# Optimization experiments

Measured on AMD Instinct MI355X. Metric: run time of the kernel, lower is better.

Reference implementation:

```python
import jax, jax.numpy as jnp
import numpy as np

D_MODEL = 1024
EXPANDED = 1024  # d_model * expansion_factor(1.0)
K = 3
EPS = 1e-8


def rms_norm(x, w, eps=EPS):
    return x * jax.lax.rsqrt(jnp.mean(x * x, axis=-1, keepdims=True) + eps) * w


def setup_inputs() -> dict:
    key = jax.random.key(0)
    ks = jax.random.split(key, 8)
    b, t = 4, 4096
    u = jax.random.normal(ks[0], (b, t, D_MODEL), dtype=jnp.float32)
    s_in = 1.0 / np.sqrt(D_MODEL)
    s_out = 1.0 / np.sqrt(EXPANDED)
    W_in = jax.random.uniform(ks[1], (2 * EXPANDED, D_MODEL), jnp.float32, -s_in, s_in)
    b_in = jax.random.uniform(ks[2], (2 * EXPANDED,), jnp.float32, -s_in, s_in)
    in_norm_w = jnp.ones((2 * EXPANDED,), jnp.float32)
    s_conv = 1.0 / np.sqrt(K)  # groups=expanded_dim -> fan_in = K
    conv_w = jax.random.uniform(ks[3], (EXPANDED, 1, K), jnp.float32, -s_conv, s_conv)
    conv_b = jax.random.uniform(ks[4], (EXPANDED,), jnp.float32, -s_conv, s_conv)
    W_out = jax.random.uniform(ks[5], (D_MODEL, EXPANDED), jnp.float32, -s_out, s_out)
    b_out = jax.random.uniform(ks[6], (D_MODEL,), jnp.float32, -s_out, s_out)
    out_norm_w = jnp.ones((D_MODEL,), jnp.float32)
    return {
        "u": u, "W_in": W_in, "b_in": b_in, "in_norm_w": in_norm_w,
        "conv_w": conv_w, "conv_b": conv_b,
        "W_out": W_out, "b_out": b_out, "out_norm_w": out_norm_w,
    }


def reference(u, W_in, b_in, in_norm_w, conv_w, conv_b, W_out, b_out, out_norm_w):
    # in_proj + RMSNorm
    xv = rms_norm(jnp.einsum('btd,ed->bte', u, W_in) + b_in, in_norm_w)  # [b,t,2E]
    x, v = jnp.split(xv, 2, axis=-1)  # each [b,t,E]
    # depthwise 'same' conv along time: NCH layout
    x_f = jnp.transpose(x, (0, 2, 1))  # [b,E,t]
    pad = (K - 1) // 2
    y = jax.lax.conv_general_dilated(
        x_f, conv_w, window_strides=(1,), padding=[(pad, pad)],
        dimension_numbers=('NCH', 'OIH', 'NCH'), feature_group_count=EXPANDED)
    y = y + conv_b[None, :, None]
    x_mixed = jnp.transpose(y, (0, 2, 1))  # [b,t,E]
    gated = v * x_mixed
    out = rms_norm(jnp.einsum('bte,de->btd', gated, W_out) + b_out, out_norm_w)
    return out
```

## Files before the change

kernel.cpp:

```cpp
#include <hip/hip_runtime.h>

#define BT    16384
#define TSEQ  4096
#define DM    1024
#define EXP   1024
#define N1    2048
#define KDIM  1024
#define NKT   32
#define EPSV  1e-8f

typedef __bf16 bf16x8 __attribute__((ext_vector_type(8)));
typedef float f32x16 __attribute__((ext_vector_type(16)));
typedef unsigned short u16x8 __attribute__((ext_vector_type(8)));

#define AS1CAST(p) ((__attribute__((address_space(1))) void*)(p))
#define AS3CAST(p) ((__attribute__((address_space(3))) void*)(p))

__device__ __forceinline__ unsigned short f2bf(float f) {
    unsigned int u = __float_as_uint(f);
    u += 0x7fffu + ((u >> 16) & 1u);
    return (unsigned short)(u >> 16);
}

__global__ __launch_bounds__(256) void k_f2bf3(const float* __restrict__ i0, unsigned short* __restrict__ o0, int n0,
                                               const float* __restrict__ i1, unsigned short* __restrict__ o1, int n1,
                                               const float* __restrict__ i2, unsigned short* __restrict__ o2, int n2,
                                               float* __restrict__ ssq) {
    int i = blockIdx.x * 256 + threadIdx.x;
    const float* in; unsigned short* out;
    if (i < n0)                { in = i0; out = o0; }
    else if (i < n0 + n1)      { in = i1; out = o1; i -= n0; }
    else if (i < n0 + n1 + n2) { in = i2; out = o2; i -= n0 + n1; }
    else {
        i -= n0 + n1 + n2;
        if (i < 2 * BT / 4) ((float4*)ssq)[i] = make_float4(0.f, 0.f, 0.f, 0.f);
        return;
    }
    float4 v = ((const float4*)in)[i];
    ushort4 o;
    o.x = f2bf(v.x); o.y = f2bf(v.y); o.z = f2bf(v.z); o.w = f2bf(v.w);
    ((ushort4*)out)[i] = o;
}

template <int BF16_OUT, int NT>
__device__ __forceinline__ void gemm_body(const unsigned short* __restrict__ A,
                                          const unsigned short* __restrict__ Bw,
                                          const float* __restrict__ bias,
                                          unsigned short* __restrict__ Cb,
                                          float* __restrict__ Cf,
                                          float* __restrict__ ssq,
                                          int N) {
    __shared__ __align__(16) char smem[73728];

    const int tid  = threadIdx.x;
    const int lane = tid & 63;
    const int w    = tid >> 6;
    const int ln   = lane & 31;
    const int hi   = lane >> 5;

    const int L   = blockIdx.x;
    const int mt  = ((L >> 3) / NT) * 8 + (L & 7);
    const int nt  = (L >> 3) & (NT - 1);
    const int row0 = mt * 256, col0 = nt * 128;

    const int rA = tid >> 2;
    const int qS = ((tid & 3) - (tid >> 4)) & 3;
    const unsigned short* aSrc = A  + (size_t)(row0 + rA) * KDIM + qS * 8;
    const unsigned short* bSrc = Bw + (size_t)(col0 + rA) * KDIM + qS * 8;

    f32x16 acc[2][4] = {};

    auto stage = [&](int kt, unsigned short* sA, unsigned short* sB) {
#pragma unroll
        for (int b = 0; b < 4; ++b)
            __builtin_amdgcn_global_load_lds(AS1CAST(aSrc + (size_t)b * 64 * KDIM + kt * 32),
                                             AS3CAST(&sA[(b * 256 + w * 64) * 8]), 16, 0, 0);
#pragma unroll
        for (int b = 0; b < 2; ++b)
            __builtin_amdgcn_global_load_lds(AS1CAST(bSrc + (size_t)b * 64 * KDIM + kt * 32),
                                             AS3CAST(&sB[(b * 256 + w * 64) * 8]), 16, 0, 0);
    };
    auto compute = [&](const unsigned short* sA, const unsigned short* sB) {
#pragma unroll
        for (int ks = 0; ks < 2; ++ks) {
            const int sw = ((ks * 2 + hi + (ln >> 2)) & 3) * 8;
            bf16x8 aF[2], bF[4];
#pragma unroll
            for (int i = 0; i < 2; ++i)
                aF[i] = *(const bf16x8*)&sA[(w * 64 + i * 32 + ln) * 32 + sw];
#pragma unroll
            for (int j = 0; j < 4; ++j)
                bF[j] = *(const bf16x8*)&sB[(j * 32 + ln) * 32 + sw];
            __builtin_amdgcn_s_setprio(1);
#pragma unroll
            for (int i = 0; i < 2; ++i)
#pragma unroll
                for (int j = 0; j < 4; ++j)
                    acc[i][j] = __builtin_amdgcn_mfma_f32_32x32x16_bf16(
                        aF[i], bF[j], acc[i][j], 0, 0, 0);
            __builtin_amdgcn_s_setprio(0);
        }
    };

    unsigned short* A0 = (unsigned short*)smem;
    unsigned short* B0 = (unsigned short*)(smem + 16384);
    unsigned short* A1 = (unsigned short*)(smem + 24576);
    unsigned short* B1 = (unsigned short*)(smem + 40960);
    unsigned short* A2 = (unsigned short*)(smem + 49152);
    unsigned short* B2 = (unsigned short*)(smem + 65536);

    stage(0, A0, B0);
    stage(1, A1, B1);
    for (int kt = 0; kt < NKT - 1; ++kt) {
        asm volatile("s_waitcnt vmcnt(6)" ::: "memory");
        __builtin_amdgcn_s_barrier();
        if (kt + 2 < NKT) stage(kt + 2, A2, B2);
        compute(A0, B0);
        unsigned short* tA = A0; A0 = A1; A1 = A2; A2 = tA;
        unsigned short* tB = B0; B0 = B1; B1 = B2; B2 = tB;
    }
    asm volatile("s_waitcnt vmcnt(0)" ::: "memory");
    __builtin_amdgcn_s_barrier();
    compute(A0, B0);

    const int c0 = col0 + ln;
    float bs[4];
#pragma unroll
    for (int j = 0; j < 4; ++j) bs[j] = bias[c0 + j * 32];

    __syncthreads();
    float* scr = (float*)smem;

#pragma unroll
    for (int i = 0; i < 2; ++i) {
        const int lr0 = w * 64 + i * 32 + 4 * hi;
#pragma unroll
        for (int reg = 0; reg < 16; ++reg) {
            const int lr = lr0 + (reg & 3) + 8 * (reg >> 2);
            const int gm = row0 + lr;
            float v[4]; float p = 0.f;
#pragma unroll
            for (int j = 0; j < 4; ++j) {
                v[j] = acc[i][j][reg] + bs[j];
                p += v[j] * v[j];
            }
            scr[lr * 33 + ln] = p;
            size_t base = (size_t)gm * N + c0;
#pragma unroll
            for (int j = 0; j < 4; ++j) {
                if (BF16_OUT) Cb[base + j * 32] = f2bf(v[j]);
                else          Cf[base + j * 32] = v[j];
            }
        }
    }
    __syncthreads();
    float s = 0.f;
#pragma unroll
    for (int c = 0; c < 32; ++c) s += scr[tid * 33 + c];
    atomicAdd(&ssq[row0 + tid], s);
}

__global__ __launch_bounds__(256, 2) void k_gemm_in(const unsigned short* __restrict__ A,
                                                    const unsigned short* __restrict__ Bw,
                                                    const float* __restrict__ bias,
                                                    unsigned short* __restrict__ Cb,
                                                    float* __restrict__ ssq) {
    gemm_body<1, 16>(A, Bw, bias, Cb, nullptr, ssq, N1);
}

__global__ __launch_bounds__(256, 2) void k_gemm_out(const unsigned short* __restrict__ A,
                                                     const unsigned short* __restrict__ Bw,
                                                     const float* __restrict__ bias,
                                                     float* __restrict__ Cf,
                                                     float* __restrict__ ssq) {
    gemm_body<0, 8>(A, Bw, bias, nullptr, Cf, ssq, DM);
}

__global__ __launch_bounds__(256) void k_conv_gate(const unsigned short* __restrict__ z,
                                                   const float* __restrict__ ssq1,
                                                   const float* __restrict__ inw,
                                                   const float* __restrict__ cw,
                                                   const float* __restrict__ cb,
                                                   unsigned short* __restrict__ g) {
    const int tok = blockIdx.x * 2 + (threadIdx.x >> 7);
    const int e8  = (threadIdx.x & 127) * 8;
    const int t   = tok & (TSEQ - 1);

    const float rs0 = rsqrtf(ssq1[tok] * (1.0f / N1) + EPSV);
    const int tm = (t > 0) ? tok - 1 : tok;
    const int tp = (t < TSEQ - 1) ? tok + 1 : tok;
    const float rsm = (t > 0) ? rsqrtf(ssq1[tm] * (1.0f / N1) + EPSV) : 0.0f;
    const float rsp = (t < TSEQ - 1) ? rsqrtf(ssq1[tp] * (1.0f / N1) + EPSV) : 0.0f;

    bf16x8 xm = *(const bf16x8*)(z + (size_t)tm * N1 + e8);
    bf16x8 x0 = *(const bf16x8*)(z + (size_t)tok * N1 + e8);
    bf16x8 xp = *(const bf16x8*)(z + (size_t)tp * N1 + e8);
    bf16x8 vv = *(const bf16x8*)(z + (size_t)tok * N1 + EXP + e8);

    u16x8 ov;
#pragma unroll
    for (int p = 0; p < 8; ++p) {
        const int e = e8 + p;
        const float we  = inw[e];
        const float wvv = inw[EXP + e];
        const float w0 = cw[e * 3], w1 = cw[e * 3 + 1], w2 = cw[e * 3 + 2];
        float y = w0 * ((float)xm[p] * rsm * we)
                + w1 * ((float)x0[p] * rs0 * we)
                + w2 * ((float)xp[p] * rsp * we)
                + cb[e];
        float vn = (float)vv[p] * rs0 * wvv;
        ov[p] = f2bf(vn * y);
    }
    *(u16x8*)(g + (size_t)tok * EXP + e8) = ov;
}

__global__ __launch_bounds__(256) void k_outnorm(float* __restrict__ o,
                                                 const float* __restrict__ ssq2,
                                                 const float* __restrict__ onw) {
    const int idx = blockIdx.x * 256 + threadIdx.x;
    const int tok = idx >> 8;
    const int d4  = (idx & 255) * 4;
    const float rs = rsqrtf(ssq2[tok] * (1.0f / DM) + EPSV);
    float4 v = ((float4*)o)[idx];
    float4 w = *(const float4*)(onw + d4);
    v.x *= rs * w.x; v.y *= rs * w.y; v.z *= rs * w.z; v.w *= rs * w.w;
    ((float4*)o)[idx] = v;
}

extern "C" void kernel_launch(void* const* d_in, const int* in_sizes, int n_in,
                              void* d_out, int out_size, void* d_ws, size_t ws_size,
                              hipStream_t stream) {
    const float* u     = (const float*)d_in[0];
    const float* W_in  = (const float*)d_in[1];
    const float* b_in  = (const float*)d_in[2];
    const float* inw   = (const float*)d_in[3];
    const float* cw    = (const float*)d_in[4];
    const float* cb    = (const float*)d_in[5];
    const float* W_out = (const float*)d_in[6];
    const float* b_out = (const float*)d_in[7];
    const float* onw   = (const float*)d_in[8];
    float* out = (float*)d_out;

    char* ws = (char*)d_ws;
    unsigned short* u_bf    = (unsigned short*)ws; ws += (size_t)BT * DM * 2;
    unsigned short* Win_bf  = (unsigned short*)ws; ws += (size_t)N1 * DM * 2;
    unsigned short* Wout_bf = (unsigned short*)ws; ws += (size_t)DM * EXP * 2;
    unsigned short* z_bf    = (unsigned short*)ws; ws += (size_t)BT * N1 * 2;
    unsigned short* g_bf    = (unsigned short*)ws; ws += (size_t)BT * EXP * 2;
    float* ssq1 = (float*)ws; ws += (size_t)BT * 4;
    float* ssq2 = (float*)ws; ws += (size_t)BT * 4;

    const int n0 = BT * DM / 4, n1c = N1 * DM / 4, n2c = DM * EXP / 4;
    const int ntot = n0 + n1c + n2c + 2 * BT / 4;
    k_f2bf3<<<(ntot + 255) / 256, 256, 0, stream>>>(u, u_bf, n0,
                                                    W_in, Win_bf, n1c,
                                                    W_out, Wout_bf, n2c,
                                                    ssq1);

    k_gemm_in<<<(BT / 256) * (N1 / 128), 256, 0, stream>>>(u_bf, Win_bf, b_in, z_bf, ssq1);

    k_conv_gate<<<BT / 2, 256, 0, stream>>>(z_bf, ssq1, inw, cw, cb, g_bf);

    k_gemm_out<<<(BT / 256) * (DM / 128), 256, 0, stream>>>(g_bf, Wout_bf, b_out, out, ssq2);

    k_outnorm<<<BT, 256, 0, stream>>>(out, ssq2, onw);

    (void)in_sizes; (void)n_in; (void)out_size; (void)ws_size;
}
```

Measured before the change: 299.6 us.

## Restructure GEMMs to 256x256 tiles with 8 waves and 16x16 MFMA

Both projection GEMMs move from 256x128 tiles on 4 waves to 256x256 tiles on 8 waves (512 threads), using 16x16x32 bf16 MFMAs and a 64-wide K step. Each K step is split into two halves whose global-to-LDS loads are interleaved with MFMA phases, with barriers between phases and a new XOR swizzle. The row sum-of-squares reduction now uses lane shuffles and per-row atomics instead of an LDS scratch pass. Larger tiles cut global and LDS traffic per flop, but the 128 KB of LDS and high register use limit occupancy and add more barriers.

After: 301.9 us. No clear change (+0.8%).

```diff
diff --git a/kernel.cpp b/kernel.cpp
--- a/kernel.cpp
+++ b/kernel.cpp
@@ -6,11 +6,11 @@
 #define EXP   1024
 #define N1    2048
 #define KDIM  1024
-#define NKT   32
+#define NKT   16
 #define EPSV  1e-8f
 
 typedef __bf16 bf16x8 __attribute__((ext_vector_type(8)));
-typedef float f32x16 __attribute__((ext_vector_type(16)));
+typedef float f32x4 __attribute__((ext_vector_type(4)));
 typedef unsigned short u16x8 __attribute__((ext_vector_type(8)));
 
 #define AS1CAST(p) ((__attribute__((address_space(1))) void*)(p))
@@ -42,7 +42,7 @@
     ((ushort4*)out)[i] = o;
 }
 
-template <int BF16_OUT, int NT>
+template <int BF16_OUT, int NTN>
 __device__ __forceinline__ void gemm_body(const unsigned short* __restrict__ A,
                                           const unsigned short* __restrict__ Bw,
                                           const float* __restrict__ bias,
@@ -50,130 +50,165 @@
                                           float* __restrict__ Cf,
                                           float* __restrict__ ssq,
                                           int N) {
-    __shared__ __align__(16) char smem[73728];
+    __shared__ __align__(16) char smem[131072];
 
     const int tid  = threadIdx.x;
     const int lane = tid & 63;
     const int w    = tid >> 6;
-    const int ln   = lane & 31;
-    const int hi   = lane >> 5;
+    const int wm   = w >> 2;
+    const int wn   = w & 3;
+    const int l15  = lane & 15;
+    const int l4   = lane >> 4;
 
     const int L   = blockIdx.x;
-    const int mt  = ((L >> 3) / NT) * 8 + (L & 7);
-    const int nt  = (L >> 3) & (NT - 1);
-    const int row0 = mt * 256, col0 = nt * 128;
-
-    const int rA = tid >> 2;
-    const int qS = ((tid & 3) - (tid >> 4)) & 3;
-    const unsigned short* aSrc = A  + (size_t)(row0 + rA) * KDIM + qS * 8;
-    const unsigned short* bSrc = Bw + (size_t)(col0 + rA) * KDIM + qS * 8;
-
-    f32x16 acc[2][4] = {};
-
-    auto stage = [&](int kt, unsigned short* sA, unsigned short* sB) {
-#pragma unroll
-        for (int b = 0; b < 4; ++b)
-            __builtin_amdgcn_global_load_lds(AS1CAST(aSrc + (size_t)b * 64 * KDIM + kt * 32),
-                                             AS3CAST(&sA[(b * 256 + w * 64) * 8]), 16, 0, 0);
+    const int cpx = (NTN * (BT / 256)) >> 3;
+    const int W   = (L & 7) * cpx + (L >> 3);
+    const int mt  = W / NTN, nt = W % NTN;
+    const int row0 = mt * 256, col0 = nt * 256;
+
+    const int rS = tid >> 2;
+    const int qS = (tid & 3) ^ ((tid >> 3) & 3);
+
+    auto stageA = [&](int T2, int kh) {
+        const unsigned short* src = A + (size_t)(row0 + rS) * KDIM + T2 * 64 + kh * 32 + qS * 8;
+        char* dst = smem + ((T2 & 1) * 32768 + kh * 16384) + tid * 16;
 #pragma unroll
         for (int b = 0; b < 2; ++b)
-            __builtin_amdgcn_global_load_lds(AS1CAST(bSrc + (size_t)b * 64 * KDIM + kt * 32),
-                                             AS3CAST(&sB[(b * 256 + w * 64) * 8]), 16, 0, 0);
+            __builtin_amdgcn_global_load_lds(AS1CAST(src + (size_t)b * 128 * KDIM),
+                                             AS3CAST(dst + b * 8192), 16, 0, 0);
     };
-    auto compute = [&](const unsigned short* sA, const unsigned short* sB) {
-#pragma unroll
-        for (int ks = 0; ks < 2; ++ks) {
-            const int sw = ((ks * 2 + hi + (ln >> 2)) & 3) * 8;
-            bf16x8 aF[2], bF[4];
-#pragma unroll
-            for (int i = 0; i < 2; ++i)
-                aF[i] = *(const bf16x8*)&sA[(w * 64 + i * 32 + ln) * 32 + sw];
-#pragma unroll
-            for (int j = 0; j < 4; ++j)
-                bF[j] = *(const bf16x8*)&sB[(j * 32 + ln) * 32 + sw];
-            __builtin_amdgcn_s_setprio(1);
-#pragma unroll
-            for (int i = 0; i < 2; ++i)
-#pragma unroll
-                for (int j = 0; j < 4; ++j)
-                    acc[i][j] = __builtin_amdgcn_mfma_f32_32x32x16_bf16(
-                        aF[i], bF[j], acc[i][j], 0, 0, 0);
-            __builtin_amdgcn_s_setprio(0);
-        }
+    auto stageB = [&](int T2, int kh) {
+        const unsigned short* src = Bw + (size_t)(col0 + rS) * KDIM + T2 * 64 + kh * 32 + qS * 8;
+        char* dst = smem + (65536 + (T2 & 1) * 32768 + kh * 16384) + tid * 16;
+#pragma unroll
+        for (int b = 0; b < 2; ++b)
+            __builtin_amdgcn_global_load_lds(AS1CAST(src + (size_t)b * 128 * KDIM),
+                                             AS3CAST(dst + b * 8192), 16, 0, 0);
     };
 
-    unsigned short* A0 = (unsigned short*)smem;
-    unsigned short* B0 = (unsigned short*)(smem + 16384);
-    unsigned short* A1 = (unsigned short*)(smem + 24576);
-    unsigned short* B1 = (unsigned short*)(smem + 40960);
-    unsigned short* A2 = (unsigned short*)(smem + 49152);
-    unsigned short* B2 = (unsigned short*)(smem + 65536);
-
-    stage(0, A0, B0);
-    stage(1, A1, B1);
-    for (int kt = 0; kt < NKT - 1; ++kt) {
-        asm volatile("s_waitcnt vmcnt(6)" ::: "memory");
-        __builtin_amdgcn_s_barrier();
-        if (kt + 2 < NKT) stage(kt + 2, A2, B2);
-        compute(A0, B0);
-        unsigned short* tA = A0; A0 = A1; A1 = A2; A2 = tA;
-        unsigned short* tB = B0; B0 = B1; B1 = B2; B2 = tB;
+    const int pslot = (l4 ^ ((l15 >> 1) & 3)) * 16;
+    const int aL = (wm * 128 + l15) * 64 + pslot;
+    const int bL = (wn * 64 + l15) * 64 + pslot;
+
+    f32x4 acc[8][4] = {};
+
+    stageA(0, 0); stageB(0, 0);
+    stageA(0, 1); stageB(0, 1);
+    stageA(1, 0); stageB(1, 0);
+    asm volatile("s_waitcnt vmcnt(4)" ::: "memory");
+    __builtin_amdgcn_s_barrier();
+
+#pragma unroll 1
+    for (int T = 0; T < NKT; ++T) {
+        const char* Ab = smem + (T & 1) * 32768;
+        const char* Bb = smem + 65536 + (T & 1) * 32768;
+        bf16x8 aF[8], bF[4];
+
+#pragma unroll
+        for (int mr = 0; mr < 8; ++mr) aF[mr] = *(const bf16x8*)(Ab + aL + mr * 1024);
+        bF[0] = *(const bf16x8*)(Bb + bL);
+        bF[1] = *(const bf16x8*)(Bb + bL + 1024);
+        if (T + 1 < NKT) stageA(T + 1, 1);
+        __builtin_amdgcn_s_barrier();
+        asm volatile("s_waitcnt lgkmcnt(0)" ::: "memory");
+        __builtin_amdgcn_s_setprio(1);
+#pragma unroll
+        for (int mr = 0; mr < 8; ++mr) {
+            acc[mr][0] = __builtin_amdgcn_mfma_f32_16x16x32_bf16(aF[mr], bF[0], acc[mr][0], 0, 0, 0);
+            acc[mr][1] = __builtin_amdgcn_mfma_f32_16x16x32_bf16(aF[mr], bF[1], acc[mr][1], 0, 0, 0);
+        }
+        __builtin_amdgcn_s_setprio(0);
+        __builtin_amdgcn_s_barrier();
+
+        bF[2] = *(const bf16x8*)(Bb + bL + 2048);
+        bF[3] = *(const bf16x8*)(Bb + bL + 3072);
+        if (T + 1 < NKT) stageB(T + 1, 1);
+        __builtin_amdgcn_s_barrier();
+        asm volatile("s_waitcnt lgkmcnt(0)" ::: "memory");
+        __builtin_amdgcn_s_setprio(1);
+#pragma unroll
+        for (int mr = 0; mr < 8; ++mr) {
+            acc[mr][2] = __builtin_amdgcn_mfma_f32_16x16x32_bf16(aF[mr], bF[2], acc[mr][2], 0, 0, 0);
+            acc[mr][3] = __builtin_amdgcn_mfma_f32_16x16x32_bf16(aF[mr], bF[3], acc[mr][3], 0, 0, 0);
+        }
+        __builtin_amdgcn_s_setprio(0);
+        __builtin_amdgcn_s_barrier();
+
+#pragma unroll
+        for (int mr = 0; mr < 8; ++mr) aF[mr] = *(const bf16x8*)(Ab + 16384 + aL + mr * 1024);
+        bF[0] = *(const bf16x8*)(Bb + 16384 + bL);
+        bF[1] = *(const bf16x8*)(Bb + 16384 + bL + 1024);
+        if (T + 2 < NKT) stageA(T + 2, 0);
+        __builtin_amdgcn_s_barrier();
+        asm volatile("s_waitcnt lgkmcnt(0)" ::: "memory");
+        __builtin_amdgcn_s_setprio(1);
+#pragma unroll
+        for (int mr = 0; mr < 8; ++mr) {
+            acc[mr][0] = __builtin_amdgcn_mfma_f32_16x16x32_bf16(aF[mr], bF[0], acc[mr][0], 0, 0, 0);
+            acc[mr][1] = __builtin_amdgcn_mfma_f32_16x16x32_bf16(aF[mr], bF[1], acc[mr][1], 0, 0, 0);
+        }
+        __builtin_amdgcn_s_setprio(0);
+        __builtin_amdgcn_s_barrier();
+
+        bF[2] = *(const bf16x8*)(Bb + 16384 + bL + 2048);
+        bF[3] = *(const bf16x8*)(Bb + 16384 + bL + 3072);
+        if (T + 2 < NKT) stageB(T + 2, 0);
+        __builtin_amdgcn_s_barrier();
+        asm volatile("s_waitcnt lgkmcnt(0)" ::: "memory");
+        __builtin_amdgcn_s_setprio(1);
+#pragma unroll
+        for (int mr = 0; mr < 8; ++mr) {
+            acc[mr][2] = __builtin_amdgcn_mfma_f32_16x16x32_bf16(aF[mr], bF[2], acc[mr][2], 0, 0, 0);
+            acc[mr][3] = __builtin_amdgcn_mfma_f32_16x16x32_bf16(aF[mr], bF[3], acc[mr][3], 0, 0, 0);
+        }
+        __builtin_amdgcn_s_setprio(0);
+        if (T < NKT - 2) asm volatile("s_waitcnt vmcnt(4)" ::: "memory");
+        else             asm volatile("s_waitcnt vmcnt(0)" ::: "memory");
+        __builtin_amdgcn_s_barrier();
     }
-    asm volatile("s_waitcnt vmcnt(0)" ::: "memory");
-    __builtin_amdgcn_s_barrier();
-    compute(A0, B0);
-
-    const int c0 = col0 + ln;
-    float bs[4];
-#pragma unroll
-    for (int j = 0; j < 4; ++j) bs[j] = bias[c0 + j * 32];
-
-    __syncthreads();
-    float* scr = (float*)smem;
-
-#pragma unroll
-    for (int i = 0; i < 2; ++i) {
-        const int lr0 = w * 64 + i * 32 + 4 * hi;
-#pragma unroll
-        for (int reg = 0; reg < 16; ++reg) {
-            const int lr = lr0 + (reg & 3) + 8 * (reg >> 2);
-            const int gm = row0 + lr;
-            float v[4]; float p = 0.f;
-#pragma unroll
-            for (int j = 0; j < 4; ++j) {
-                v[j] = acc[i][j][reg] + bs[j];
-                p += v[j] * v[j];
+
+    const int c0 = col0 + wn * 64 + l15;
+    float bsv[4];
+#pragma unroll
+    for (int nr = 0; nr < 4; ++nr) bsv[nr] = bias[c0 + nr * 16];
+
+#pragma unroll
+    for (int mr = 0; mr < 8; ++mr) {
+#pragma unroll
+        for (int reg = 0; reg < 4; ++reg) {
+            const int gm = row0 + wm * 128 + mr * 16 + l4 * 4 + reg;
+            const size_t base = (size_t)gm * N + c0;
+            float p = 0.f;
+#pragma unroll
+            for (int nr = 0; nr < 4; ++nr) {
+                float v = acc[mr][nr][reg] + bsv[nr];
+                p += v * v;
+                if (BF16_OUT) Cb[base + nr * 16] = f2bf(v);
+                else          Cf[base + nr * 16] = v;
             }
-            scr[lr * 33 + ln] = p;
-            size_t base = (size_t)gm * N + c0;
-#pragma unroll
-            for (int j = 0; j < 4; ++j) {
-                if (BF16_OUT) Cb[base + j * 32] = f2bf(v[j]);
-                else          Cf[base + j * 32] = v[j];
-            }
+            p += __shfl_xor(p, 1);
+            p += __shfl_xor(p, 2);
+            p += __shfl_xor(p, 4);
+            p += __shfl_xor(p, 8);
+            if (l15 == 0) atomicAdd(&ssq[gm], p);
         }
     }
-    __syncthreads();
-    float s = 0.f;
-#pragma unroll
-    for (int c = 0; c < 32; ++c) s += scr[tid * 33 + c];
-    atomicAdd(&ssq[row0 + tid], s);
-}
-
-__global__ __launch_bounds__(256, 2) void k_gemm_in(const unsigned short* __restrict__ A,
+}
+
+__global__ __launch_bounds__(512, 2) void k_gemm_in(const unsigned short* __restrict__ A,
                                                     const unsigned short* __restrict__ Bw,
                                                     const float* __restrict__ bias,
                                                     unsigned short* __restrict__ Cb,
                                                     float* __restrict__ ssq) {
-    gemm_body<1, 16>(A, Bw, bias, Cb, nullptr, ssq, N1);
-}
-
-__global__ __launch_bounds__(256, 2) void k_gemm_out(const unsigned short* __restrict__ A,
+    gemm_body<1, 8>(A, Bw, bias, Cb, nullptr, ssq, N1);
+}
+
+__global__ __launch_bounds__(512, 2) void k_gemm_out(const unsigned short* __restrict__ A,
                                                      const unsigned short* __restrict__ Bw,
                                                      const float* __restrict__ bias,
                                                      float* __restrict__ Cf,
                                                      float* __restrict__ ssq) {
-    gemm_body<0, 8>(A, Bw, bias, nullptr, Cf, ssq, DM);
+    gemm_body<0, 4>(A, Bw, bias, nullptr, Cf, ssq, DM);
 }
 
 __global__ __launch_bounds__(256) void k_conv_gate(const unsigned short* __restrict__ z,
@@ -257,11 +292,11 @@
                                                     W_out, Wout_bf, n2c,
                                                     ssq1);
 
-    k_gemm_in<<<(BT / 256) * (N1 / 128), 256, 0, stream>>>(u_bf, Win_bf, b_in, z_bf, ssq1);
+    k_gemm_in<<<(BT / 256) * (N1 / 256), 512, 0, stream>>>(u_bf, Win_bf, b_in, z_bf, ssq1);
 
     k_conv_gate<<<BT / 2, 256, 0, stream>>>(z_bf, ssq1, inw, cw, cb, g_bf);
 
-    k_gemm_out<<<(BT / 256) * (DM / 128), 256, 0, stream>>>(g_bf, Wout_bf, b_out, out, ssq2);
+    k_gemm_out<<<(BT / 256) * (DM / 256), 512, 0, stream>>>(g_bf, Wout_bf, b_out, out, ssq2);
 
     k_outnorm<<<BT, 256, 0, stream>>>(out, ssq2, onw);
 
```

## Fuse output RMSNorm into a full-row output GEMM kernel

Applied to the files above, without the earlier changes.

Replaces the tiled output GEMM, its atomic sum-of-squares accumulation and the separate output-norm pass with one kernel. Each 512-thread block computes 64 complete rows across all 1024 output columns and reduces the row norms in shared memory before writing the normalized result once. This removes a full fp32 read/write pass over the output, the atomics and one launch. In exchange every block streams all of W_out from L2, uses about 136KB of LDS (one block per CU) and drops to a double-buffered pipeline that waits on all loads each step.

Result: slower. 305.9 us (+2.1%).

```diff
diff --git a/kernel.cpp b/kernel.cpp
--- a/kernel.cpp
+++ b/kernel.cpp
@@ -6,7 +6,7 @@
 #define EXP   1024
 #define N1    2048
 #define KDIM  1024
-#define NKT   32
+#define NKT2  (KDIM / 32)
 #define EPSV  1e-8f
 
 typedef __bf16 bf16x8 __attribute__((ext_vector_type(8)));
@@ -33,7 +33,7 @@
     else if (i < n0 + n1 + n2) { in = i2; out = o2; i -= n0 + n1; }
     else {
         i -= n0 + n1 + n2;
-        if (i < 2 * BT / 4) ((float4*)ssq)[i] = make_float4(0.f, 0.f, 0.f, 0.f);
+        if (i < BT / 4) ((float4*)ssq)[i] = make_float4(0.f, 0.f, 0.f, 0.f);
         return;
     }
     float4 v = ((const float4*)in)[i];
@@ -111,10 +111,10 @@
 
     stage(0, A0, B0);
     stage(1, A1, B1);
-    for (int kt = 0; kt < NKT - 1; ++kt) {
+    for (int kt = 0; kt < NKT2 - 1; ++kt) {
         asm volatile("s_waitcnt vmcnt(6)" ::: "memory");
         __builtin_amdgcn_s_barrier();
-        if (kt + 2 < NKT) stage(kt + 2, A2, B2);
+        if (kt + 2 < NKT2) stage(kt + 2, A2, B2);
         compute(A0, B0);
         unsigned short* tA = A0; A0 = A1; A1 = A2; A2 = tA;
         unsigned short* tB = B0; B0 = B1; B1 = B2; B2 = tB;
@@ -168,12 +168,122 @@
     gemm_body<1, 16>(A, Bw, bias, Cb, nullptr, ssq, N1);
 }
 
-__global__ __launch_bounds__(256, 2) void k_gemm_out(const unsigned short* __restrict__ A,
-                                                     const unsigned short* __restrict__ Bw,
-                                                     const float* __restrict__ bias,
-                                                     float* __restrict__ Cf,
-                                                     float* __restrict__ ssq) {
-    gemm_body<0, 8>(A, Bw, bias, nullptr, Cf, ssq, DM);
+__global__ __launch_bounds__(512, 2) void k_gemm_outn(const unsigned short* __restrict__ A,
+                                                      const unsigned short* __restrict__ Bw,
+                                                      const float* __restrict__ bias,
+                                                      const float* __restrict__ onw,
+                                                      float* __restrict__ O) {
+    __shared__ __align__(16) char smem[139264];
+
+    const int tid  = threadIdx.x;
+    const int lane = tid & 63;
+    const int w    = tid >> 6;
+    const int ln   = lane & 31;
+    const int hi   = lane >> 5;
+    const int row0 = blockIdx.x * 64;
+
+    const int rS = tid >> 2;
+    const int qS = ((tid & 3) - (tid >> 4)) & 3;
+    const unsigned short* aSrc = A  + (size_t)(row0 + (rS & 63)) * KDIM + qS * 8;
+    const unsigned short* bSrc = Bw + (size_t)rS * KDIM + qS * 8;
+
+    auto stage = [&](int kt, char* sA, char* sB) {
+        if (tid < 256)
+            __builtin_amdgcn_global_load_lds(AS1CAST(aSrc + kt * 32),
+                                             AS3CAST(sA + tid * 16), 16, 0, 0);
+#pragma unroll
+        for (int b = 0; b < 8; ++b)
+            __builtin_amdgcn_global_load_lds(AS1CAST(bSrc + (size_t)b * 128 * KDIM + kt * 32),
+                                             AS3CAST(sB + (b * 512 + tid) * 16), 16, 0, 0);
+    };
+
+    f32x16 acc[2][4] = {};
+
+    auto compute = [&](const char* sAc, const char* sBc) {
+        const unsigned short* sA = (const unsigned short*)sAc;
+        const unsigned short* sB = (const unsigned short*)sBc;
+#pragma unroll
+        for (int ks = 0; ks < 2; ++ks) {
+            const int sw = ((ks * 2 + hi + (ln >> 2)) & 3) * 8;
+            bf16x8 aF[2], bF[4];
+#pragma unroll
+            for (int i = 0; i < 2; ++i)
+                aF[i] = *(const bf16x8*)&sA[(i * 32 + ln) * 32 + sw];
+#pragma unroll
+            for (int j = 0; j < 4; ++j)
+                bF[j] = *(const bf16x8*)&sB[(w * 128 + j * 32 + ln) * 32 + sw];
+            __builtin_amdgcn_s_setprio(1);
+#pragma unroll
+            for (int i = 0; i < 2; ++i)
+#pragma unroll
+                for (int j = 0; j < 4; ++j)
+                    acc[i][j] = __builtin_amdgcn_mfma_f32_32x32x16_bf16(
+                        aF[i], bF[j], acc[i][j], 0, 0, 0);
+            __builtin_amdgcn_s_setprio(0);
+        }
+    };
+
+    char* A0 = smem;          char* B0 = smem + 4096;
+    char* A1 = smem + 69632;  char* B1 = smem + 73728;
+
+    stage(0, A0, B0);
+#pragma unroll 1
+    for (int T = 0; T < NKT2; ++T) {
+        asm volatile("s_waitcnt vmcnt(0)" ::: "memory");
+        __builtin_amdgcn_s_barrier();
+        if (T + 1 < NKT2) stage(T + 1, (T & 1) ? A0 : A1, (T & 1) ? B0 : B1);
+        compute((T & 1) ? A1 : A0, (T & 1) ? B1 : B0);
+    }
+
+    __syncthreads();
+    float* part = (float*)smem;
+
+    const int c0 = w * 128 + ln;
+    float bs[4], wn[4];
+#pragma unroll
+    for (int j = 0; j < 4; ++j) { bs[j] = bias[c0 + j * 32]; wn[j] = onw[c0 + j * 32]; }
+
+#pragma unroll
+    for (int i = 0; i < 2; ++i) {
+#pragma unroll
+        for (int reg = 0; reg < 16; ++reg) {
+            const int r = i * 32 + (reg & 3) + 8 * (reg >> 2) + 4 * hi;
+            float p = 0.f;
+#pragma unroll
+            for (int j = 0; j < 4; ++j) {
+                float v = acc[i][j][reg] + bs[j];
+                p += v * v;
+            }
+            p += __shfl_xor(p, 1);
+            p += __shfl_xor(p, 2);
+            p += __shfl_xor(p, 4);
+            p += __shfl_xor(p, 8);
+            p += __shfl_xor(p, 16);
+            if (ln == 0) part[r * 8 + w] = p;
+        }
+    }
+    __syncthreads();
+    if (tid < 64) {
+        float s = 0.f;
+#pragma unroll
+        for (int k = 0; k < 8; ++k) s += part[tid * 8 + k];
+        part[512 + tid] = rsqrtf(s * (1.0f / DM) + EPSV);
+    }
+    __syncthreads();
+    const float* rsv = part + 512;
+
+#pragma unroll
+    for (int i = 0; i < 2; ++i) {
+#pragma unroll
+        for (int reg = 0; reg < 16; ++reg) {
+            const int r = i * 32 + (reg & 3) + 8 * (reg >> 2) + 4 * hi;
+            const float rf = rsv[r];
+            const size_t base = (size_t)(row0 + r) * DM + c0;
+#pragma unroll
+            for (int j = 0; j < 4; ++j)
+                O[base + j * 32] = (acc[i][j][reg] + bs[j]) * rf * wn[j];
+        }
+    }
 }
 
 __global__ __launch_bounds__(256) void k_conv_gate(const unsigned short* __restrict__ z,
@@ -212,19 +322,6 @@
         ov[p] = f2bf(vn * y);
     }
     *(u16x8*)(g + (size_t)tok * EXP + e8) = ov;
-}
-
-__global__ __launch_bounds__(256) void k_outnorm(float* __restrict__ o,
-                                                 const float* __restrict__ ssq2,
-                                                 const float* __restrict__ onw) {
-    const int idx = blockIdx.x * 256 + threadIdx.x;
-    const int tok = idx >> 8;
-    const int d4  = (idx & 255) * 4;
-    const float rs = rsqrtf(ssq2[tok] * (1.0f / DM) + EPSV);
-    float4 v = ((float4*)o)[idx];
-    float4 w = *(const float4*)(onw + d4);
-    v.x *= rs * w.x; v.y *= rs * w.y; v.z *= rs * w.z; v.w *= rs * w.w;
-    ((float4*)o)[idx] = v;
 }
 
 extern "C" void kernel_launch(void* const* d_in, const int* in_sizes, int n_in,
@@ -248,10 +345,9 @@
     unsigned short* z_bf    = (unsigned short*)ws; ws += (size_t)BT * N1 * 2;
     unsigned short* g_bf    = (unsigned short*)ws; ws += (size_t)BT * EXP * 2;
     float* ssq1 = (float*)ws; ws += (size_t)BT * 4;
-    float* ssq2 = (float*)ws; ws += (size_t)BT * 4;
 
     const int n0 = BT * DM / 4, n1c = N1 * DM / 4, n2c = DM * EXP / 4;
-    const int ntot = n0 + n1c + n2c + 2 * BT / 4;
+    const int ntot = n0 + n1c + n2c + BT / 4;
     k_f2bf3<<<(ntot + 255) / 256, 256, 0, stream>>>(u, u_bf, n0,
                                                     W_in, Win_bf, n1c,
                                                     W_out, Wout_bf, n2c,
@@ -261,9 +357,7 @@
 
     k_conv_gate<<<BT / 2, 256, 0, stream>>>(z_bf, ssq1, inw, cw, cb, g_bf);
 
-    k_gemm_out<<<(BT / 256) * (DM / 128), 256, 0, stream>>>(g_bf, Wout_bf, b_out, out, ssq2);
-
-    k_outnorm<<<BT, 256, 0, stream>>>(out, ssq2, onw);
+    k_gemm_outn<<<BT / 64, 512, 0, stream>>>(g_bf, Wout_bf, b_out, onw, out);
 
     (void)in_sizes; (void)n_in; (void)out_size; (void)ws_size;
 }
```

## Fuse output RMSNorm into out-GEMM via last-block counter and remap conv blocks

Applied to the files above, without the earlier changes.

Removes the separate output-norm kernel. Each out-GEMM block bumps a per-row-tile atomic counter, and the last of the 8 column blocks for a 256-row tile reads the finished sum of squares and rescales that tile's rows in place. The counter array is zeroed alongside ssq in the conversion kernel. The conv_gate block index is also permuted so neighbouring blocks are spread across 8 groups, probably to improve XCD/cache locality. This saves a launch and one pass over the output, but the whole normalization of a tile now falls on a single block, and the out-GEMM's tile-to-block mapping has to match the mt formula used here.

Result: slower. 477.6 us (+59.4%).

```diff
diff --git a/kernel.cpp b/kernel.cpp
--- a/kernel.cpp
+++ b/kernel.cpp
@@ -6,7 +6,7 @@
 #define EXP   1024
 #define N1    2048
 #define KDIM  1024
-#define NKT   32
+#define NKT2  (KDIM / 32)
 #define EPSV  1e-8f
 
 typedef __bf16 bf16x8 __attribute__((ext_vector_type(8)));
@@ -33,7 +33,7 @@
     else if (i < n0 + n1 + n2) { in = i2; out = o2; i -= n0 + n1; }
     else {
         i -= n0 + n1 + n2;
-        if (i < 2 * BT / 4) ((float4*)ssq)[i] = make_float4(0.f, 0.f, 0.f, 0.f);
+        if (i < (2 * BT + 64) / 4) ((float4*)ssq)[i] = make_float4(0.f, 0.f, 0.f, 0.f);
         return;
     }
     float4 v = ((const float4*)in)[i];
@@ -111,10 +111,10 @@
 
     stage(0, A0, B0);
     stage(1, A1, B1);
-    for (int kt = 0; kt < NKT - 1; ++kt) {
+    for (int kt = 0; kt < NKT2 - 1; ++kt) {
         asm volatile("s_waitcnt vmcnt(6)" ::: "memory");
         __builtin_amdgcn_s_barrier();
-        if (kt + 2 < NKT) stage(kt + 2, A2, B2);
+        if (kt + 2 < NKT2) stage(kt + 2, A2, B2);
         compute(A0, B0);
         unsigned short* tA = A0; A0 = A1; A1 = A2; A2 = tA;
         unsigned short* tB = B0; B0 = B1; B1 = B2; B2 = tB;
@@ -172,8 +172,37 @@
                                                      const unsigned short* __restrict__ Bw,
                                                      const float* __restrict__ bias,
                                                      float* __restrict__ Cf,
-                                                     float* __restrict__ ssq) {
+                                                     float* __restrict__ ssq,
+                                                     const float* __restrict__ onw,
+                                                     int* __restrict__ cnt) {
     gemm_body<0, 8>(A, Bw, bias, nullptr, Cf, ssq, DM);
+
+    const int L   = blockIdx.x;
+    const int mt  = ((L >> 3) / 8) * 8 + (L & 7);
+    const int row0 = mt * 256;
+
+    __shared__ int done;
+    __shared__ float rsbuf[256];
+
+    __threadfence();
+    if (threadIdx.x == 0) done = atomicAdd(&cnt[mt], 1);
+    __syncthreads();
+    if (done != 7) return;
+
+    __threadfence();
+    rsbuf[threadIdx.x] = rsqrtf(ssq[row0 + threadIdx.x] * (1.0f / DM) + EPSV);
+    __syncthreads();
+
+    const float4 wv = ((const float4*)onw)[threadIdx.x];
+    float4* Of = (float4*)Cf;
+#pragma unroll 4
+    for (int r = 0; r < 256; ++r) {
+        const float rs = rsbuf[r];
+        const size_t idx = (size_t)(row0 + r) * 256 + threadIdx.x;
+        float4 v = Of[idx];
+        v.x *= rs * wv.x; v.y *= rs * wv.y; v.z *= rs * wv.z; v.w *= rs * wv.w;
+        Of[idx] = v;
+    }
 }
 
 __global__ __launch_bounds__(256) void k_conv_gate(const unsigned short* __restrict__ z,
@@ -182,7 +211,9 @@
                                                    const float* __restrict__ cw,
                                                    const float* __restrict__ cb,
                                                    unsigned short* __restrict__ g) {
-    const int tok = blockIdx.x * 2 + (threadIdx.x >> 7);
+    const int L   = blockIdx.x;
+    const int blk = (L & 7) * 1024 + (L >> 3);
+    const int tok = blk * 2 + (threadIdx.x >> 7);
     const int e8  = (threadIdx.x & 127) * 8;
     const int t   = tok & (TSEQ - 1);
 
@@ -212,19 +243,6 @@
         ov[p] = f2bf(vn * y);
     }
     *(u16x8*)(g + (size_t)tok * EXP + e8) = ov;
-}
-
-__global__ __launch_bounds__(256) void k_outnorm(float* __restrict__ o,
-                                                 const float* __restrict__ ssq2,
-                                                 const float* __restrict__ onw) {
-    const int idx = blockIdx.x * 256 + threadIdx.x;
-    const int tok = idx >> 8;
-    const int d4  = (idx & 255) * 4;
-    const float rs = rsqrtf(ssq2[tok] * (1.0f / DM) + EPSV);
-    float4 v = ((float4*)o)[idx];
-    float4 w = *(const float4*)(onw + d4);
-    v.x *= rs * w.x; v.y *= rs * w.y; v.z *= rs * w.z; v.w *= rs * w.w;
-    ((float4*)o)[idx] = v;
 }
 
 extern "C" void kernel_launch(void* const* d_in, const int* in_sizes, int n_in,
@@ -249,9 +267,10 @@
     unsigned short* g_bf    = (unsigned short*)ws; ws += (size_t)BT * EXP * 2;
     float* ssq1 = (float*)ws; ws += (size_t)BT * 4;
     float* ssq2 = (float*)ws; ws += (size_t)BT * 4;
+    int*   cnt  = (int*)ws;  ws += 64 * 4;
 
     const int n0 = BT * DM / 4, n1c = N1 * DM / 4, n2c = DM * EXP / 4;
-    const int ntot = n0 + n1c + n2c + 2 * BT / 4;
+    const int ntot = n0 + n1c + n2c + (2 * BT + 64) / 4;
     k_f2bf3<<<(ntot + 255) / 256, 256, 0, stream>>>(u, u_bf, n0,
                                                     W_in, Win_bf, n1c,
                                                     W_out, Wout_bf, n2c,
@@ -261,9 +280,7 @@
 
     k_conv_gate<<<BT / 2, 256, 0, stream>>>(z_bf, ssq1, inw, cw, cb, g_bf);
 
-    k_gemm_out<<<(BT / 256) * (DM / 128), 256, 0, stream>>>(g_bf, Wout_bf, b_out, out, ssq2);
-
-    k_outnorm<<<BT, 256, 0, stream>>>(out, ssq2, onw);
+    k_gemm_out<<<(BT / 256) * (DM / 128), 256, 0, stream>>>(g_bf, Wout_bf, b_out, out, ssq2, onw, cnt);
 
     (void)in_sizes; (void)n_in; (void)out_size; (void)ws_size;
 }
```
